# Kernel optimization log

Hardware: AMD Instinct MI355X
Metric: run time of the kernel (lower is better)

Reference implementation:

```python
import jax, jax.numpy as jnp
import numpy as np

N_NODES = 100000
N_EDGES = 1600000
D_IN = 128
D_OUT = 128


def setup_inputs() -> dict:
    key = jax.random.key(0)
    k1, k2, k3, k4, k5 = jax.random.split(key, 5)
    x = jax.random.normal(k1, (N_NODES, D_IN), dtype=jnp.float32)
    edge_index = jax.random.randint(k2, (2, N_EDGES), 0, N_NODES, dtype=jnp.int32)
    edge_weight = jax.random.uniform(k3, (N_EDGES,), dtype=jnp.float32)
    # xavier-uniform linear weight [out, in]
    limit = float(np.sqrt(6.0 / (D_IN + D_OUT)))
    W = jax.random.uniform(k4, (D_OUT, D_IN), dtype=jnp.float32, minval=-limit, maxval=limit)
    bias = jnp.zeros((D_OUT,), dtype=jnp.float32)
    prelu_a = jax.random.uniform(k5, (1,), dtype=jnp.float32)
    return {"x": x, "edge_index": edge_index, "edge_weight": edge_weight,
            "W": W, "bias": bias, "prelu_a": prelu_a}


def _prelu(x, a):
    return jnp.where(x >= 0, x, a * x)


def reference(x, edge_index, edge_weight, W, bias, prelu_a):
    # seq_fts = fc(x): [N, D_OUT]
    h = x @ W.T
    # sparse adjacency matmul: out[dst] += w_e * h[src]
    src, dst = edge_index[0], edge_index[1]
    msgs = h[src] * edge_weight[:, None]          # [E, D_OUT]
    agg = jax.ops.segment_sum(msgs, dst, num_segments=N_NODES)
    out = agg + bias                              # bias add
    out = _prelu(out, prelu_a)                    # GCN's PReLU
    return jax.nn.relu(out)                       # GCNGeneration.activation
```

## Files before the change

kernel.cpp:

```cpp
#include <hip/hip_runtime.h>

#define N_NODES 100000
#define N_EDGES 1600000
#define D 128

#define NCB   512
#define BR    196
#define CHUNK 8192
#define SLOTS 24
#define CAP   6144

#define XQ   (N_NODES * D / 4)
#define XQB  (XQ / 256)
#define WQ   (D * D / 4)
#define WQB  (WQ / 256)
#define HB   256

typedef __bf16 bf16x8 __attribute__((ext_vector_type(8)));
typedef float  f32x4  __attribute__((ext_vector_type(4)));
typedef unsigned short u16x8 __attribute__((ext_vector_type(8)));

static __device__ __forceinline__ unsigned short f2bf(float f) {
    union { float f; unsigned u; } v; v.f = f;
    unsigned r = v.u + 0x7FFFu + ((v.u >> 16) & 1u);
    return (unsigned short)(r >> 16);
}

static __device__ __forceinline__ void accum_row(
    float4& acc0, float4& acc1, const float4 u, const float wt)
{
    const unsigned qx = __float_as_uint(u.x);
    const unsigned qy = __float_as_uint(u.y);
    const unsigned qz = __float_as_uint(u.z);
    const unsigned qw = __float_as_uint(u.w);
    acc0.x += wt * __uint_as_float(qx << 16);
    acc0.y += wt * __uint_as_float(qx & 0xFFFF0000u);
    acc0.z += wt * __uint_as_float(qy << 16);
    acc0.w += wt * __uint_as_float(qy & 0xFFFF0000u);
    acc1.x += wt * __uint_as_float(qz << 16);
    acc1.y += wt * __uint_as_float(qz & 0xFFFF0000u);
    acc1.z += wt * __uint_as_float(qw << 16);
    acc1.w += wt * __uint_as_float(qw & 0xFFFF0000u);
}

__global__ __launch_bounds__(256) void k_prep(
    const float4* __restrict__ x4, ushort4* __restrict__ xh4,
    const float4* __restrict__ w4, ushort4* __restrict__ wh4,
    const int* __restrict__ ei, int* __restrict__ hpart)
{
    __shared__ int h[NCB];
    const int b = blockIdx.x;
    const int t = threadIdx.x;
    if (b < HB) {
        h[t] = 0; h[t + 256] = 0;
        __syncthreads();
        for (int e = b * 256 + t; e < N_EDGES; e += HB * 256)
            atomicAdd(&h[ei[N_EDGES + e] / BR], 1);
        __syncthreads();
        hpart[b * NCB + t]       = h[t];
        hpart[b * NCB + t + 256] = h[t + 256];
    } else if (b < HB + XQB) {
        const int i = (b - HB) * 256 + t;
        const float4 v = x4[i];
        xh4[i] = make_ushort4(f2bf(v.x), f2bf(v.y), f2bf(v.z), f2bf(v.w));
    } else {
        const int i = (b - HB - XQB) * 256 + t;
        const float4 v = w4[i];
        wh4[i] = make_ushort4(f2bf(v.x), f2bf(v.y), f2bf(v.z), f2bf(v.w));
    }
}

__global__ __launch_bounds__(512) void k_cscan(
    const int* __restrict__ hpart, int* __restrict__ cOff, int* __restrict__ gcur)
{
    __shared__ int sh[NCB];
    const int t = threadIdx.x;
    int v = 0;
    #pragma unroll 8
    for (int k = 0; k < HB; ++k) v += hpart[k * NCB + t];
    sh[t] = v;
    __syncthreads();
    for (int d = 1; d < NCB; d <<= 1) {
        int u = (t >= d) ? sh[t - d] : 0;
        __syncthreads();
        sh[t] += u;
        __syncthreads();
    }
    const int excl = sh[t] - v;
    cOff[t] = excl;
    gcur[t] = excl;
    if (t == NCB - 1) cOff[NCB] = sh[NCB - 1];
}

__global__ __launch_bounds__(256, 1) void k_part(
    const int* __restrict__ ei, const float* __restrict__ ew,
    int* __restrict__ gcur, int2* __restrict__ part)
{
    __shared__ int2 bins[NCB * SLOTS];
    __shared__ int bcnt[NCB];
    __shared__ int bbase[NCB];
    const int t = threadIdx.x;
    const int e0 = blockIdx.x * CHUNK;

    bcnt[t] = 0; bcnt[t + 256] = 0;
    __syncthreads();

    #pragma unroll 8
    for (int k = 0; k < CHUNK / 256; ++k) {
        const int e = e0 + k * 256 + t;
        if (e < N_EDGES) {
            const int dst = ei[N_EDGES + e];
            const int src = ei[e];
            const int b = dst / BR;
            const int ld = dst - b * BR;
            const int2 p = make_int2(src | (ld << 17), __float_as_int(ew[e]));
            const int r = atomicAdd(&bcnt[b], 1);
            if (r < SLOTS) bins[b * SLOTS + r] = p;
            else {
                int pos = atomicAdd(&gcur[b], 1);
                part[pos] = p;
            }
        }
    }
    __syncthreads();

    {
        int c0 = min(bcnt[t], SLOTS);
        int c1 = min(bcnt[t + 256], SLOTS);
        bbase[t]       = c0 ? atomicAdd(&gcur[t], c0) : 0;
        bbase[t + 256] = c1 ? atomicAdd(&gcur[t + 256], c1) : 0;
        bcnt[t] = c0; bcnt[t + 256] = c1;
    }
    __syncthreads();

    for (int s = t; s < NCB * SLOTS; s += 256) {
        const int b = s / SLOTS;
        const int r = s - b * SLOTS;
        if (r < bcnt[b]) part[bbase[b] + r] = bins[s];
    }
}

__global__ __launch_bounds__(256) void k_csr(
    const int* __restrict__ cOff, int2* __restrict__ part, int* __restrict__ off)
{
    __shared__ int2 buf[CAP];
    __shared__ int nh[256];
    __shared__ int orig[256];
    __shared__ int cur[256];

    const int b = blockIdx.x;
    const int t = threadIdx.x;
    const int lo = b * BR;
    const int base = cOff[b];
    int cnt = cOff[b + 1] - base;
    if (cnt > CAP) cnt = CAP;

    nh[t] = 0;
    __syncthreads();

    for (int i = t; i < cnt; i += 256) {
        const int2 p = part[base + i];
        buf[i] = p;
        atomicAdd(&nh[((unsigned)p.x) >> 17], 1);
    }
    __syncthreads();
    orig[t] = nh[t];
    __syncthreads();
    for (int d = 1; d < 256; d <<= 1) {
        int u = (t >= d) ? nh[t - d] : 0;
        __syncthreads();
        nh[t] += u;
        __syncthreads();
    }
    const int excl = nh[t] - orig[t];
    cur[t] = excl;
    if (t < BR && lo + t < N_NODES) off[lo + t] = base + excl;
    if (b == NCB - 1 && t == 0) off[N_NODES] = cOff[NCB];
    __syncthreads();

    for (int i = t; i < cnt; i += 256) {
        const int2 p = buf[i];
        const int ld = ((unsigned)p.x) >> 17;
        const int r = atomicAdd(&cur[ld], 1);
        part[base + r] = make_int2(p.x & 0x1FFFF, p.y);
    }
}

__global__ __launch_bounds__(256) void k_gx(
    const float4* __restrict__ xh4,
    const int* __restrict__ off,
    const int2* __restrict__ pair,
    const unsigned short* __restrict__ wh,
    const float* __restrict__ bias, const float* __restrict__ pa,
    float* __restrict__ out)
{
    __shared__ unsigned short tb[16][136];

    const int tid = threadIdx.x;
    const int wv = tid >> 6;
    const int lane = tid & 63;
    const int grp = lane >> 4;
    const int sl = lane & 15;
    const int m0 = blockIdx.x << 4;
    const float aP = pa[0];

    for (int j = 0; j < 4; ++j) {
        const int r = (wv << 2) + j;
        const int n = m0 + r;
        const int beg = off[n], end = off[n + 1];
        float4 acc0 = make_float4(0.f, 0.f, 0.f, 0.f);
        float4 acc1 = make_float4(0.f, 0.f, 0.f, 0.f);

        int e = beg + grp;
        for (; e + 12 < end; e += 16) {
            const int2 p0 = pair[e + 0], p1 = pair[e + 4];
            const int2 p2 = pair[e + 8], p3 = pair[e + 12];
            const float4 u0 = xh4[p0.x * 16 + sl];
            const float4 u1 = xh4[p1.x * 16 + sl];
            const float4 u2 = xh4[p2.x * 16 + sl];
            const float4 u3 = xh4[p3.x * 16 + sl];
            accum_row(acc0, acc1, u0, __int_as_float(p0.y));
            accum_row(acc0, acc1, u1, __int_as_float(p1.y));
            accum_row(acc0, acc1, u2, __int_as_float(p2.y));
            accum_row(acc0, acc1, u3, __int_as_float(p3.y));
        }
        for (; e < end; e += 4) {
            const int2 p = pair[e];
            const float4 u = xh4[p.x * 16 + sl];
            accum_row(acc0, acc1, u, __int_as_float(p.y));
        }
        acc0.x += __shfl_down(acc0.x, 16, 64); acc0.y += __shfl_down(acc0.y, 16, 64);
        acc0.z += __shfl_down(acc0.z, 16, 64); acc0.w += __shfl_down(acc0.w, 16, 64);
        acc1.x += __shfl_down(acc1.x, 16, 64); acc1.y += __shfl_down(acc1.y, 16, 64);
        acc1.z += __shfl_down(acc1.z, 16, 64); acc1.w += __shfl_down(acc1.w, 16, 64);
        acc0.x += __shfl_down(acc0.x, 32, 64); acc0.y += __shfl_down(acc0.y, 32, 64);
        acc0.z += __shfl_down(acc0.z, 32, 64); acc0.w += __shfl_down(acc0.w, 32, 64);
        acc1.x += __shfl_down(acc1.x, 32, 64); acc1.y += __shfl_down(acc1.y, 32, 64);
        acc1.z += __shfl_down(acc1.z, 32, 64); acc1.w += __shfl_down(acc1.w, 32, 64);
        if (grp == 0) {
            u16x8 s;
            s[0] = f2bf(acc0.x); s[1] = f2bf(acc0.y);
            s[2] = f2bf(acc0.z); s[3] = f2bf(acc0.w);
            s[4] = f2bf(acc1.x); s[5] = f2bf(acc1.y);
            s[6] = f2bf(acc1.z); s[7] = f2bf(acc1.w);
            *(u16x8*)&tb[r][sl * 8] = s;
        }
    }
    __syncthreads();

    const int mm = lane & 15;
    const int quad = lane >> 4;

    bf16x8 af[4];
    #pragma unroll
    for (int c = 0; c < 4; ++c)
        af[c] = *(const bf16x8*)&tb[mm][c * 32 + quad * 8];

    #pragma unroll
    for (int t = 0; t < 2; ++t) {
        const int n = ((wv * 2 + t) << 4) + mm;
        f32x4 acc = {0.f, 0.f, 0.f, 0.f};
        #pragma unroll
        for (int c = 0; c < 4; ++c) {
            const bf16x8 bf = *(const bf16x8*)(wh + n * D + c * 32 + quad * 8);
            acc = __builtin_amdgcn_mfma_f32_16x16x32_bf16(af[c], bf, acc, 0, 0, 0);
        }
        const float bv = bias[n];
        #pragma unroll
        for (int r = 0; r < 4; ++r) {
            float v = acc[r] + bv;
            v = (v >= 0.f) ? v : aP * v;
            v = fmaxf(v, 0.f);
            out[(size_t)(m0 + (quad << 2) + r) * D + n] = v;
        }
    }
}

__global__ __launch_bounds__(256) void gcn_scatter(
    const float* __restrict__ x, const int* __restrict__ ei,
    const float* __restrict__ ew, float* __restrict__ agg)
{
    const int lane = threadIdx.x & 63;
    const int wave = (blockIdx.x * blockDim.x + threadIdx.x) >> 6;
    const int nwaves = (gridDim.x * blockDim.x) >> 6;
    for (int e = wave; e < N_EDGES; e += nwaves) {
        const int src = ei[e];
        const int dst = ei[N_EDGES + e];
        const float w = ew[e];
        const float2 v = ((const float2*)(x + (size_t)src * D))[lane];
        float* op = agg + (size_t)dst * D + lane * 2;
        unsafeAtomicAdd(op,     w * v.x);
        unsafeAtomicAdd(op + 1, w * v.y);
    }
}

#define MT 32
__global__ __launch_bounds__(256, 2) void gcn_transform(
    const float* __restrict__ A, const float* __restrict__ W,
    const float* __restrict__ bias, const float* __restrict__ pa,
    float* __restrict__ out)
{
    __shared__ float Wt[D][D];
    __shared__ float xs[MT][D];
    const int tid = threadIdx.x;
    const int row0 = blockIdx.x * MT;

    for (int j = tid; j < D * (D / 4); j += 256) {
        const int n = j & 127;
        const int kg = j >> 7;
        const float4 v = ((const float4*)W)[n * (D / 4) + kg];
        const int k4 = kg << 2;
        Wt[k4 + 0][n] = v.x; Wt[k4 + 1][n] = v.y;
        Wt[k4 + 2][n] = v.z; Wt[k4 + 3][n] = v.w;
    }
    for (int i = tid; i < MT * (D / 4); i += 256) {
        const int r = i >> 5;
        const int c4 = i & 31;
        ((float4*)xs[r])[c4] = ((const float4*)(A + (size_t)(row0 + r) * D))[c4];
    }
    __syncthreads();

    const int tn = tid & 31;
    const int tm = tid >> 5;
    float acc[4][4] = {};
    #pragma unroll
    for (int k = 0; k < D; k += 4) {
        const float4 wv0 = *(const float4*)&Wt[k + 0][tn * 4];
        const float4 wv1 = *(const float4*)&Wt[k + 1][tn * 4];
        const float4 wv2 = *(const float4*)&Wt[k + 2][tn * 4];
        const float4 wv3 = *(const float4*)&Wt[k + 3][tn * 4];
        #pragma unroll
        for (int i = 0; i < 4; ++i) {
            const float4 xv = *(const float4*)&xs[tm * 4 + i][k];
            acc[i][0] += xv.x * wv0.x + xv.y * wv1.x + xv.z * wv2.x + xv.w * wv3.x;
            acc[i][1] += xv.x * wv0.y + xv.y * wv1.y + xv.z * wv2.y + xv.w * wv3.y;
            acc[i][2] += xv.x * wv0.z + xv.y * wv1.z + xv.z * wv2.z + xv.w * wv3.z;
            acc[i][3] += xv.x * wv0.w + xv.y * wv1.w + xv.z * wv2.w + xv.w * wv3.w;
        }
    }
    const float a = pa[0];
    const float4 bv = ((const float4*)bias)[tn];
    #pragma unroll
    for (int i = 0; i < 4; ++i) {
        const int gr = row0 + tm * 4 + i;
        float t0 = acc[i][0] + bv.x, t1 = acc[i][1] + bv.y;
        float t2 = acc[i][2] + bv.z, t3 = acc[i][3] + bv.w;
        float4 r;
        r.x = fmaxf(t0 >= 0.f ? t0 : a * t0, 0.f);
        r.y = fmaxf(t1 >= 0.f ? t1 : a * t1, 0.f);
        r.z = fmaxf(t2 >= 0.f ? t2 : a * t2, 0.f);
        r.w = fmaxf(t3 >= 0.f ? t3 : a * t3, 0.f);
        ((float4*)(out + (size_t)gr * D))[tn] = r;
    }
}

extern "C" void kernel_launch(void* const* d_in, const int* in_sizes, int n_in,
                              void* d_out, int out_size, void* d_ws, size_t ws_size,
                              hipStream_t stream) {
    const float* x    = (const float*)d_in[0];
    const int*   ei   = (const int*)d_in[1];
    const float* ew   = (const float*)d_in[2];
    const float* W    = (const float*)d_in[3];
    const float* bias = (const float*)d_in[4];
    const float* pa   = (const float*)d_in[5];
    float* out = (float*)d_out;

    const size_t o_ghist = 0;
    const size_t o_cOff  = o_ghist + NCB;
    const size_t o_gcur  = o_cOff + NCB + 1;
    const size_t o_off   = o_gcur + NCB;
    const size_t o_part  = o_off + N_NODES + 1;
    const size_t o_wh    = (o_part + 2 * (size_t)N_EDGES + 3) & ~(size_t)3;
    const size_t o_xh    = o_wh + (size_t)D * D / 2;
    const size_t endA    = o_xh + (size_t)N_NODES * D / 2;
    const size_t needA   = endA * 4;

    int* wsb = (int*)d_ws;
    int* cOff  = wsb + o_cOff;
    int* gcur  = wsb + o_gcur;
    int* off   = wsb + o_off;
    int2* part = (int2*)(wsb + o_part);
    unsigned short* wh = (unsigned short*)(wsb + o_wh);
    unsigned short* xh = (unsigned short*)(wsb + o_xh);
    int* hpart = (int*)part;

    if (ws_size >= needA) {
        k_prep <<<HB + XQB + WQB, 256, 0, stream>>>(
            (const float4*)x, (ushort4*)xh, (const float4*)W, (ushort4*)wh, ei, hpart);
        k_cscan<<<1, NCB, 0, stream>>>(hpart, cOff, gcur);
        k_part <<<(N_EDGES + CHUNK - 1) / CHUNK, 256, 0, stream>>>(ei, ew, gcur, part);
        k_csr  <<<NCB, 256, 0, stream>>>(cOff, part, off);
        k_gx   <<<N_NODES / 16, 256, 0, stream>>>(
            (const float4*)xh, off, part, wh, bias, pa, out);
    } else {
        (void)hipMemsetAsync(out, 0, (size_t)N_NODES * D * sizeof(float), stream);
        gcn_scatter<<<12800, 256, 0, stream>>>(x, ei, ew, out);
        gcn_transform<<<N_NODES / MT, 256, 0, stream>>>(out, W, bias, pa, out);
    }
}
```

Before: 278.8 us.

## Replace bucketed two-pass CSR build with per-node degree count and atomic scatter

Swaps the coarse-bucket partition plus per-bucket local sort for a direct CSR build. It counts degree per node with global atomics, runs a single-block 1024-thread scan over 100k nodes, then scatters each edge with an atomic on its destination cursor. This removes two kernels and the shared-memory binning, but it adds heavy global atomic traffic, uncoalesced scatter writes and a serial single-block scan. It also makes edge order within each node nondeterministic.

```diff
diff --git a/kernel.cpp b/kernel.cpp
--- a/kernel.cpp
+++ b/kernel.cpp
@@ -3,12 +3,6 @@
 #define N_NODES 100000
 #define N_EDGES 1600000
 #define D 128
-
-#define NCB   512
-#define BR    196
-#define CHUNK 8192
-#define SLOTS 24
-#define CAP   6144
 
 #define XQ   (N_NODES * D / 4)
 #define XQB  (XQ / 256)
@@ -46,19 +40,13 @@
 __global__ __launch_bounds__(256) void k_prep(
     const float4* __restrict__ x4, ushort4* __restrict__ xh4,
     const float4* __restrict__ w4, ushort4* __restrict__ wh4,
-    const int* __restrict__ ei, int* __restrict__ hpart)
-{
-    __shared__ int h[NCB];
+    const int* __restrict__ ei, int* __restrict__ deg)
+{
     const int b = blockIdx.x;
     const int t = threadIdx.x;
     if (b < HB) {
-        h[t] = 0; h[t + 256] = 0;
-        __syncthreads();
         for (int e = b * 256 + t; e < N_EDGES; e += HB * 256)
-            atomicAdd(&h[ei[N_EDGES + e] / BR], 1);
-        __syncthreads();
-        hpart[b * NCB + t]       = h[t];
-        hpart[b * NCB + t + 256] = h[t + 256];
+            atomicAdd(&deg[ei[N_EDGES + e]], 1);
     } else if (b < HB + XQB) {
         const int i = (b - HB) * 256 + t;
         const float4 v = x4[i];
@@ -70,119 +58,44 @@
     }
 }
 
-__global__ __launch_bounds__(512) void k_cscan(
-    const int* __restrict__ hpart, int* __restrict__ cOff, int* __restrict__ gcur)
-{
-    __shared__ int sh[NCB];
+#define SCHUNK 98
+__global__ __launch_bounds__(1024) void k_scan(
+    const int* __restrict__ deg, int* __restrict__ off, int* __restrict__ cur)
+{
+    __shared__ int sh[1024];
     const int t = threadIdx.x;
-    int v = 0;
-    #pragma unroll 8
-    for (int k = 0; k < HB; ++k) v += hpart[k * NCB + t];
-    sh[t] = v;
+    const int lo = t * SCHUNK;
+    const int hi = min(lo + SCHUNK, N_NODES);
+    int s = 0;
+    for (int i = lo; i < hi; ++i) s += deg[i];
+    sh[t] = s;
     __syncthreads();
-    for (int d = 1; d < NCB; d <<= 1) {
+    for (int d = 1; d < 1024; d <<= 1) {
         int u = (t >= d) ? sh[t - d] : 0;
         __syncthreads();
         sh[t] += u;
         __syncthreads();
     }
-    const int excl = sh[t] - v;
-    cOff[t] = excl;
-    gcur[t] = excl;
-    if (t == NCB - 1) cOff[NCB] = sh[NCB - 1];
-}
-
-__global__ __launch_bounds__(256, 1) void k_part(
+    int running = sh[t] - s;
+    for (int i = lo; i < hi; ++i) {
+        const int dv = deg[i];
+        off[i] = running;
+        cur[i] = running;
+        running += dv;
+    }
+    if (t == 1023) off[N_NODES] = sh[1023];
+}
+
+__global__ __launch_bounds__(256) void k_scat(
     const int* __restrict__ ei, const float* __restrict__ ew,
-    int* __restrict__ gcur, int2* __restrict__ part)
-{
-    __shared__ int2 bins[NCB * SLOTS];
-    __shared__ int bcnt[NCB];
-    __shared__ int bbase[NCB];
-    const int t = threadIdx.x;
-    const int e0 = blockIdx.x * CHUNK;
-
-    bcnt[t] = 0; bcnt[t + 256] = 0;
-    __syncthreads();
-
-    #pragma unroll 8
-    for (int k = 0; k < CHUNK / 256; ++k) {
-        const int e = e0 + k * 256 + t;
-        if (e < N_EDGES) {
-            const int dst = ei[N_EDGES + e];
-            const int src = ei[e];
-            const int b = dst / BR;
-            const int ld = dst - b * BR;
-            const int2 p = make_int2(src | (ld << 17), __float_as_int(ew[e]));
-            const int r = atomicAdd(&bcnt[b], 1);
-            if (r < SLOTS) bins[b * SLOTS + r] = p;
-            else {
-                int pos = atomicAdd(&gcur[b], 1);
-                part[pos] = p;
-            }
-        }
-    }
-    __syncthreads();
-
-    {
-        int c0 = min(bcnt[t], SLOTS);
-        int c1 = min(bcnt[t + 256], SLOTS);
-        bbase[t]       = c0 ? atomicAdd(&gcur[t], c0) : 0;
-        bbase[t + 256] = c1 ? atomicAdd(&gcur[t + 256], c1) : 0;
-        bcnt[t] = c0; bcnt[t + 256] = c1;
-    }
-    __syncthreads();
-
-    for (int s = t; s < NCB * SLOTS; s += 256) {
-        const int b = s / SLOTS;
-        const int r = s - b * SLOTS;
-        if (r < bcnt[b]) part[bbase[b] + r] = bins[s];
-    }
-}
-
-__global__ __launch_bounds__(256) void k_csr(
-    const int* __restrict__ cOff, int2* __restrict__ part, int* __restrict__ off)
-{
-    __shared__ int2 buf[CAP];
-    __shared__ int nh[256];
-    __shared__ int orig[256];
-    __shared__ int cur[256];
-
-    const int b = blockIdx.x;
-    const int t = threadIdx.x;
-    const int lo = b * BR;
-    const int base = cOff[b];
-    int cnt = cOff[b + 1] - base;
-    if (cnt > CAP) cnt = CAP;
-
-    nh[t] = 0;
-    __syncthreads();
-
-    for (int i = t; i < cnt; i += 256) {
-        const int2 p = part[base + i];
-        buf[i] = p;
-        atomicAdd(&nh[((unsigned)p.x) >> 17], 1);
-    }
-    __syncthreads();
-    orig[t] = nh[t];
-    __syncthreads();
-    for (int d = 1; d < 256; d <<= 1) {
-        int u = (t >= d) ? nh[t - d] : 0;
-        __syncthreads();
-        nh[t] += u;
-        __syncthreads();
-    }
-    const int excl = nh[t] - orig[t];
-    cur[t] = excl;
-    if (t < BR && lo + t < N_NODES) off[lo + t] = base + excl;
-    if (b == NCB - 1 && t == 0) off[N_NODES] = cOff[NCB];
-    __syncthreads();
-
-    for (int i = t; i < cnt; i += 256) {
-        const int2 p = buf[i];
-        const int ld = ((unsigned)p.x) >> 17;
-        const int r = atomicAdd(&cur[ld], 1);
-        part[base + r] = make_int2(p.x & 0x1FFFF, p.y);
+    int* __restrict__ cur, int2* __restrict__ part)
+{
+    const int e = blockIdx.x * 256 + threadIdx.x;
+    if (e < N_EDGES) {
+        const int src = ei[e];
+        const int dst = ei[N_EDGES + e];
+        const int pos = atomicAdd(&cur[dst], 1);
+        part[pos] = make_int2(src, __float_as_int(ew[e]));
     }
 }
 
@@ -365,31 +278,28 @@
     const float* pa   = (const float*)d_in[5];
     float* out = (float*)d_out;
 
-    const size_t o_ghist = 0;
-    const size_t o_cOff  = o_ghist + NCB;
-    const size_t o_gcur  = o_cOff + NCB + 1;
-    const size_t o_off   = o_gcur + NCB;
-    const size_t o_part  = o_off + N_NODES + 1;
-    const size_t o_wh    = (o_part + 2 * (size_t)N_EDGES + 3) & ~(size_t)3;
+    const size_t o_off   = 0;
+    const size_t o_cur   = 100004;
+    const size_t o_part  = 200004;
+    const size_t o_wh    = o_part + 2 * (size_t)N_EDGES;
     const size_t o_xh    = o_wh + (size_t)D * D / 2;
     const size_t endA    = o_xh + (size_t)N_NODES * D / 2;
     const size_t needA   = endA * 4;
 
     int* wsb = (int*)d_ws;
-    int* cOff  = wsb + o_cOff;
-    int* gcur  = wsb + o_gcur;
     int* off   = wsb + o_off;
+    int* cur   = wsb + o_cur;
     int2* part = (int2*)(wsb + o_part);
     unsigned short* wh = (unsigned short*)(wsb + o_wh);
     unsigned short* xh = (unsigned short*)(wsb + o_xh);
-    int* hpart = (int*)part;
+    int* deg = (int*)part;
 
     if (ws_size >= needA) {
+        (void)hipMemsetAsync(deg, 0, N_NODES * sizeof(int), stream);
         k_prep <<<HB + XQB + WQB, 256, 0, stream>>>(
-            (const float4*)x, (ushort4*)xh, (const float4*)W, (ushort4*)wh, ei, hpart);
-        k_cscan<<<1, NCB, 0, stream>>>(hpart, cOff, gcur);
-        k_part <<<(N_EDGES + CHUNK - 1) / CHUNK, 256, 0, stream>>>(ei, ew, gcur, part);
-        k_csr  <<<NCB, 256, 0, stream>>>(cOff, part, off);
+            (const float4*)x, (ushort4*)xh, (const float4*)W, (ushort4*)wh, ei, deg);
+        k_scan <<<1, 1024, 0, stream>>>(deg, off, cur);
+        k_scat <<<(N_EDGES + 255) / 256, 256, 0, stream>>>(ei, ew, cur, part);
         k_gx   <<<N_NODES / 16, 256, 0, stream>>>(
             (const float4*)xh, off, part, wh, bias, pa, out);
     } else {
```

After: 603.4 us. +116.4%, slower.
